# Kernel optimization log

Measured on AMD Instinct MI355X. Metric: run time of the kernel, lower is better.

The kernel has to match this reference:

```python
import jax, jax.numpy as jnp
import numpy as np

BN_EPS = 1e-5


def _weight_mlp(off, Wh, bh, Wo, bo):
    # off: [Nout, k, 2] relative neighbor offsets -> [Nout, k, 9] interp coeffs
    h = jax.nn.relu(off @ Wh + bh)
    return h @ Wo + bo


def _interp_conv(x, idx, off, Wk, bk, Wh, bh, Wo, bo):
    # x: [B, Cin, Nin]; idx: [Nout, k] neighbor indices into Nin; Wk: [Cout, Cin, 9]
    a = _weight_mlp(off, Wh, bh, Wo, bo)        # [Nout, k, 9]
    feats = x[:, :, idx]                         # gather -> [B, Cin, Nout, k]
    # dynamic filter: per-neighbor kernel = a @ Wk taps, contracted with features
    y = jnp.einsum('nkt,bcnk,oct->bon', a, feats, Wk)  # [B, Cout, Nout]
    return y + bk[None, :, None]


def _bn_relu(x, g, b):
    # BatchNorm1d over [B, C, N] using batch statistics (training-mode forward)
    mean = x.mean(axis=(0, 2), keepdims=True)
    var = x.var(axis=(0, 2), keepdims=True)
    xn = (x - mean) * jax.lax.rsqrt(var + BN_EPS)
    return jax.nn.relu(xn * g[None, :, None] + b[None, :, None])


def setup_inputs() -> dict:
    key = jax.random.key(0)
    ks = jax.random.split(key, 12)
    B, N1, N2, N3, K = 8, 50176, 12544, 3136, 9
    inp = {
        'x': jax.random.normal(ks[0], (B, 3, N1), jnp.float32),
        'nbr1': jax.random.randint(ks[1], (N2, K), 0, N1, jnp.int32),
        'off1': jax.random.normal(ks[2], (N2, K, 2), jnp.float32),
        'nbr2': jax.random.randint(ks[3], (N2, K), 0, N2, jnp.int32),
        'off2': jax.random.normal(ks[4], (N2, K, 2), jnp.float32),
        'pool_idx': jax.random.randint(ks[5], (N3, K), 0, N2, jnp.int32),
        'Wh': jax.random.normal(ks[6], (2, 32), jnp.float32) * 0.5,
        'bh': jnp.zeros((32,), jnp.float32),
        'Wo': jax.random.normal(ks[7], (32, 9), jnp.float32) * 0.2,
        'bo': jnp.zeros((9,), jnp.float32),
        'W1': jax.random.normal(ks[8], (32, 3, 9), jnp.float32) * 0.2,
        'b1': jnp.zeros((32,), jnp.float32),
        'W2': jax.random.normal(ks[9], (32, 32, 9), jnp.float32) * 0.06,
        'b2': jnp.zeros((32,), jnp.float32),
        'W3': jax.random.normal(ks[10], (64, 32, 9), jnp.float32) * 0.06,
        'b3': jnp.zeros((64,), jnp.float32),
        'g1': jnp.ones((32,), jnp.float32), 'be1': jnp.zeros((32,), jnp.float32),
        'g2': jnp.ones((32,), jnp.float32), 'be2': jnp.zeros((32,), jnp.float32),
        'g3': jnp.ones((64,), jnp.float32), 'be3': jnp.zeros((64,), jnp.float32),
    }
    return inp


def reference(x, nbr1, off1, nbr2, off2, pool_idx, Wh, bh, Wo, bo,
              W1, b1, W2, b2, W3, b3, g1, be1, g2, be2, g3, be3):
    x = _bn_relu(_interp_conv(x, nbr1, off1, W1, b1, Wh, bh, Wo, bo), g1, be1)
    x = _bn_relu(_interp_conv(x, nbr2, off2, W2, b2, Wh, bh, Wo, bo), g2, be2)
    x = _bn_relu(_interp_conv(x, nbr2, off2, W3, b3, Wh, bh, Wo, bo), g3, be3)
    # MaxPoolNG: max over irregular neighbor sets from level l2 -> l3
    x = x[:, :, pool_idx].max(axis=-1)           # [B, 64, N3]
    return x
```

## Files before the change

kernel.cpp:

```cpp
#include <hip/hip_runtime.h>
#include <math.h>

#define N1C 50176
#define N2C 12544
#define N3C 3136
#define NT_TILES (N2C * 8 / 64)

typedef __attribute__((ext_vector_type(8))) short bf16x8;
typedef __attribute__((ext_vector_type(4))) float f32x4;

__device__ __forceinline__ unsigned short f2bf(float f) {
    unsigned u = __builtin_bit_cast(unsigned, f);
    u += 0x7fffu + ((u >> 16) & 1u);
    return (unsigned short)(u >> 16);
}
__device__ __forceinline__ unsigned packbf(float a, float b) {
    return (unsigned)f2bf(a) | ((unsigned)f2bf(b) << 16);
}
__device__ __forceinline__ float bf2f(unsigned short u) {
    return __builtin_bit_cast(float, (unsigned)u << 16);
}
__device__ __forceinline__ float bflo(unsigned u) {
    return __builtin_bit_cast(float, u << 16);
}
__device__ __forceinline__ float bfhi(unsigned u) {
    return __builtin_bit_cast(float, u & 0xffff0000u);
}

#define TRB (N1C / 64)
#define MLB (2 * N2C * 9 / 256)
#define PWB 112

__device__ __forceinline__ void pad_one(int i, const float* __restrict__ W,
                                        unsigned short* __restrict__ Wp,
                                        int OC, int CIN, int KT) {
    int j = i & 7;
    int op = (i >> 3) & 31;
    int q = (i >> 8) & 3;
    int kt = (i >> 10) % KT;
    int g = i / (KT * 1024);
    int kp = kt * 32 + q * 8 + j;
    int t = kp / CIN, c = kp - t * CIN;
    int o = g * 32 + op;
    float v = (t < 9 && o < OC) ? W[(o * CIN + c) * 9 + t] : 0.f;
    Wp[i] = f2bf(v);
}

__global__ void prologue_kernel(const float* __restrict__ x, unsigned short* __restrict__ X0,
                                const float* __restrict__ off1, const float* __restrict__ off2,
                                const float* __restrict__ Wh, const float* __restrict__ bh,
                                const float* __restrict__ Wo, const float* __restrict__ bo,
                                float* __restrict__ A1, float* __restrict__ A2,
                                const float* __restrict__ W1, const float* __restrict__ W2,
                                const float* __restrict__ W3,
                                unsigned short* __restrict__ W1p, unsigned short* __restrict__ W2p,
                                unsigned short* __restrict__ W3p) {
    __shared__ float T[64][25];
    int blk = blockIdx.x;
    int tid = threadIdx.x;
    if (blk < TRB) {
        int n0 = blk * 64;
        for (int r = tid; r < 24 * 64; r += 256) {
            int cb = r >> 6;
            int nn = r & 63;
            T[nn][cb] = x[cb * N1C + n0 + nn];
        }
        __syncthreads();
        for (int w = tid; w < 64 * 24; w += 256) {
            int nn = w / 24;
            int u = w - nn * 24;
            X0[(n0 + nn) * 24 + u] = f2bf(T[nn][u]);
        }
    } else if (blk < TRB + MLB) {
        int idx = (blk - TRB) * 256 + tid;
        const float* offp;
        float* Ap;
        if (idx < N2C * 9) { offp = off1 + idx * 2; Ap = A1 + idx * 9; }
        else { int i2 = idx - N2C * 9; offp = off2 + i2 * 2; Ap = A2 + i2 * 9; }
        float o0 = offp[0], o1 = offp[1];
        float out[9];
#pragma unroll
        for (int t = 0; t < 9; t++) out[t] = bo[t];
#pragma unroll
        for (int h = 0; h < 32; h++) {
            float hv = fmaxf(o0 * Wh[h] + o1 * Wh[32 + h] + bh[h], 0.f);
#pragma unroll
            for (int t = 0; t < 9; t++) out[t] += hv * Wo[h * 9 + t];
        }
#pragma unroll
        for (int t = 0; t < 9; t++) Ap[t] = out[t];
    } else {
        int i = (blk - TRB - MLB) * 256 + tid;
        if (i < 1024) pad_one(i, W1, W1p, 32, 3, 1);
        else if (i < 10240) pad_one(i - 1024, W2, W2p, 32, 32, 9);
        else pad_one(i - 10240, W3, W3p, 64, 32, 9);
    }
}

template <int CIN, int MW, bool HAS_BN>
__global__ __launch_bounds__(256, 4)
void conv_kernel(const unsigned short* __restrict__ Xin,
                 const int* __restrict__ nbr,
                 const float* __restrict__ A,
                 const unsigned short* __restrict__ Wp,
                 const float* __restrict__ bias,
                 const float* __restrict__ bnsc,
                 const float* __restrict__ bnsh,
                 unsigned short* __restrict__ Yb,
                 double* __restrict__ Part) {
    constexpr int OC = MW * 16;
    constexpr int KREAL = 9 * CIN;
    constexpr int KROW = (KREAL + 31) & ~31;
    constexpr int KT = KROW / 32;
    constexpr int KSTR = KROW + 8;
    __shared__ alignas(16) short S[64 * KSTR];

    int tid = threadIdx.x;
    int tile = blockIdx.x;
    int n0 = tile * 8;

    if constexpr (KROW != KREAL) {
        for (int i = tid; i < 64 * KSTR; i += 256) S[i] = 0;
        __syncthreads();
    }

    if constexpr (CIN == 3) {
        if (tid < 192) {
            int nsub = tid / 24;
            int u = tid - nsub * 24;
            int b = u / 3, c = u - b * 3;
            int n = n0 + nsub;
            const int* nb = nbr + n * 9;
            const float* Ar = A + n * 81;
            float s[9];
#pragma unroll
            for (int t = 0; t < 9; t++) s[t] = 0.f;
#pragma unroll
            for (int k = 0; k < 9; k++) {
                float f = bf2f(Xin[nb[k] * 24 + u]);
#pragma unroll
                for (int t = 0; t < 9; t++) s[t] = fmaf(Ar[k * 9 + t], f, s[t]);
            }
            int col = nsub * 8 + b;
#pragma unroll
            for (int t = 0; t < 9; t++) S[col * KSTR + t * 3 + c] = (short)f2bf(s[t]);
        }
    } else {
        int nhalf = __builtin_amdgcn_readfirstlane(tid >> 7);
        int rem = tid & 127;
        int b = rem >> 4, c2 = rem & 15;
        float sc0 = 1.f, sh0 = 0.f, sc1 = 1.f, sh1 = 0.f;
        if (HAS_BN) {
            sc0 = bnsc[2 * c2];     sc1 = bnsc[2 * c2 + 1];
            sh0 = bnsh[2 * c2];     sh1 = bnsh[2 * c2 + 1];
        }
        const unsigned* Xu = (const unsigned*)Xin;
        int nbase = n0 + nhalf * 4;
        unsigned fu[36];
#pragma unroll
        for (int g = 0; g < 4; g++)
#pragma unroll
            for (int k = 0; k < 9; k++) {
                int j = nbr[(nbase + g) * 9 + k];
                fu[g * 9 + k] = Xu[(size_t)j * 128 + rem];
            }
#pragma unroll
        for (int g = 0; g < 4; g++) {
            const float* Ar = A + (nbase + g) * 81;
            float s0[9], s1[9];
#pragma unroll
            for (int t = 0; t < 9; t++) { s0[t] = 0.f; s1[t] = 0.f; }
#pragma unroll
            for (int k = 0; k < 9; k++) {
                unsigned u = fu[g * 9 + k];
                float lo = bflo(u), hi = bfhi(u);
                if (HAS_BN) {
                    lo = fmaxf(fmaf(lo, sc0, sh0), 0.f);
                    hi = fmaxf(fmaf(hi, sc1, sh1), 0.f);
                }
#pragma unroll
                for (int t = 0; t < 9; t++) {
                    float a = Ar[k * 9 + t];
                    s0[t] = fmaf(a, lo, s0[t]);
                    s1[t] = fmaf(a, hi, s1[t]);
                }
            }
            int col = (nhalf * 4 + g) * 8 + b;
            unsigned* Srow = (unsigned*)&S[col * KSTR];
#pragma unroll
            for (int t = 0; t < 9; t++) Srow[t * 16 + c2] = packbf(s0[t], s1[t]);
        }
    }
    __syncthreads();

    int lane = tid & 63, wv = tid >> 6, q = lane >> 4, cl = lane & 15;
    int colg = wv * 16 + cl;

    const bf16x8* wf = (const bf16x8*)Wp;
    f32x4 acc[MW];
#pragma unroll
    for (int m = 0; m < MW; m++) acc[m] = (f32x4){0.f, 0.f, 0.f, 0.f};
#pragma unroll
    for (int kt = 0; kt < KT; kt++) {
        bf16x8 bfr = *(const bf16x8*)&S[colg * KSTR + kt * 32 + q * 8];
#pragma unroll
        for (int m = 0; m < MW; m++) {
            const bf16x8* wg = wf + (m >> 1) * (KT * 128);
            bf16x8 am = wg[(kt * 4 + q) * 32 + cl + (m & 1) * 16];
            acc[m] = __builtin_amdgcn_mfma_f32_16x16x32_bf16(am, bfr, acc[m], 0, 0, 0);
        }
    }
    __syncthreads();
    double (*redd)[2 * OC] = (double(*)[2 * OC])S;

    int C = tile * 64 + colg;
    float yv[4 * MW];
#pragma unroll
    for (int m = 0; m < MW; m++)
#pragma unroll
        for (int i = 0; i < 4; i++) {
            int o = m * 16 + q * 4 + i;
            float y = acc[m][i] + bias[o];
            yv[m * 4 + i] = y;
            Yb[(size_t)C * OC + o] = f2bf(y);
        }
#pragma unroll
    for (int r = 0; r < 4 * MW; r++) {
        double ps = (double)yv[r];
        double pq = (double)yv[r] * (double)yv[r];
#pragma unroll
        for (int d = 1; d < 16; d <<= 1) {
            ps += __shfl_xor(ps, d);
            pq += __shfl_xor(pq, d);
        }
        if (cl == 0) {
            int o = (r >> 2) * 16 + q * 4 + (r & 3);
            redd[wv][o] = ps;
            redd[wv][OC + o] = pq;
        }
    }
    __syncthreads();
    if (tid < 2 * OC) {
        double v = redd[0][tid] + redd[1][tid] + redd[2][tid] + redd[3][tid];
        Part[(size_t)tid * NT_TILES + tile] = v;
    }
}

__global__ __launch_bounds__(256, 8)
void bn_reduce(const double* __restrict__ Part,
               const float* __restrict__ g, const float* __restrict__ be,
               float* __restrict__ sc, float* __restrict__ sh, int OC) {
    int o = blockIdx.x;
    int tid = threadIdx.x;
    const double* ps = Part + (size_t)o * NT_TILES;
    const double* pq = Part + (size_t)(OC + o) * NT_TILES;
    double s = 0.0, q = 0.0;
    for (int t = tid; t < NT_TILES; t += 256) {
        s += ps[t];
        q += pq[t];
    }
#pragma unroll
    for (int d = 1; d < 64; d <<= 1) {
        s += __shfl_xor(s, d);
        q += __shfl_xor(q, d);
    }
    __shared__ double red[8];
    int wv = tid >> 6;
    if ((tid & 63) == 0) { red[wv] = s; red[4 + wv] = q; }
    __syncthreads();
    if (tid == 0) {
        double S = red[0] + red[1] + red[2] + red[3];
        double Q = red[4] + red[5] + red[6] + red[7];
        double cnt = (double)N2C * 8.0;
        double mean = S / cnt;
        double var = Q / cnt - mean * mean;
        double rs = 1.0 / sqrt(var + 1e-5);
        double scale = (double)g[o] * rs;
        sc[o] = (float)scale;
        sh[o] = (float)((double)be[o] - mean * scale);
    }
}

__global__ __launch_bounds__(512, 4)
void pool_kernel(const unsigned short* __restrict__ Y3, const int* __restrict__ pidx,
                 const float* __restrict__ sc, const float* __restrict__ sh,
                 float* __restrict__ out) {
    int m0 = blockIdx.x * 8;
    int tid = threadIdx.x;
    int o = tid & 63;
    float s = sc[o], h = sh[o];
    float mx[8];
    int jn[9];
#pragma unroll
    for (int k = 0; k < 9; k++) jn[k] = pidx[m0 * 9 + k];
#pragma unroll 1
    for (int mi = 0; mi < 8; mi++) {
        int jc[9];
#pragma unroll
        for (int k = 0; k < 9; k++) jc[k] = jn[k];
        if (mi < 7) {
#pragma unroll
            for (int k = 0; k < 9; k++) jn[k] = pidx[(m0 + mi + 1) * 9 + k];
        }
        float v0 = 0.f;
#pragma unroll
        for (int k = 0; k < 9; k++) {
            float v = bf2f(Y3[(size_t)jc[k] * 512 + tid]);
            v0 = fmaxf(v0, fmaf(v, s, h));
        }
        mx[mi] = fmaxf(v0, 0.f);
    }
    float* op = out + (size_t)tid * 3136 + m0;
#pragma unroll
    for (int mi = 0; mi < 8; mi++) op[mi] = mx[mi];
}

extern "C" void kernel_launch(void* const* d_in, const int* in_sizes, int n_in,
                              void* d_out, int out_size, void* d_ws, size_t ws_size,
                              hipStream_t stream) {
    const float* x    = (const float*)d_in[0];
    const int*   nbr1 = (const int*)d_in[1];
    const float* off1 = (const float*)d_in[2];
    const int*   nbr2 = (const int*)d_in[3];
    const float* off2 = (const float*)d_in[4];
    const int*   pidx = (const int*)d_in[5];
    const float* Wh   = (const float*)d_in[6];
    const float* bh   = (const float*)d_in[7];
    const float* Wo   = (const float*)d_in[8];
    const float* bo   = (const float*)d_in[9];
    const float* W1   = (const float*)d_in[10];
    const float* b1   = (const float*)d_in[11];
    const float* W2   = (const float*)d_in[12];
    const float* b2   = (const float*)d_in[13];
    const float* W3   = (const float*)d_in[14];
    const float* b3   = (const float*)d_in[15];
    const float* g1   = (const float*)d_in[16];
    const float* be1  = (const float*)d_in[17];
    const float* g2   = (const float*)d_in[18];
    const float* be2  = (const float*)d_in[19];
    const float* g3   = (const float*)d_in[20];
    const float* be3  = (const float*)d_in[21];

    char* ws = (char*)d_ws;
    size_t off = 0;
    auto alloc = [&](size_t bytes) -> void* {
        void* p = ws + off;
        off += (bytes + 255) & ~(size_t)255;
        return p;
    };
    unsigned short* X0b = (unsigned short*)alloc((size_t)N1C * 24 * 2);
    float* A1 = (float*)alloc((size_t)N2C * 81 * 4);
    float* A2 = (float*)alloc((size_t)N2C * 81 * 4);
    unsigned short* Y1b = (unsigned short*)alloc((size_t)N2C * 8 * 32 * 2);
    unsigned short* Y2b = (unsigned short*)alloc((size_t)N2C * 8 * 32 * 2);
    unsigned short* Y3b = (unsigned short*)alloc((size_t)N2C * 8 * 64 * 2);
    unsigned short* W1p = (unsigned short*)alloc(32 * 32 * 2);
    unsigned short* W2p = (unsigned short*)alloc(32 * 288 * 2);
    unsigned short* W3p = (unsigned short*)alloc(64 * 288 * 2);
    double* Part  = (double*)alloc((size_t)NT_TILES * 128 * 8);
    float*  scbuf = (float*)alloc(256 * 4);

    float* sc1 = scbuf;       float* sh1 = scbuf + 32;
    float* sc2 = scbuf + 64;  float* sh2 = scbuf + 96;
    float* sc3 = scbuf + 128; float* sh3 = scbuf + 192;

    prologue_kernel<<<TRB + MLB + PWB, 256, 0, stream>>>(
        x, X0b, off1, off2, Wh, bh, Wo, bo, A1, A2, W1, W2, W3, W1p, W2p, W3p);

    conv_kernel<3, 2, false><<<NT_TILES, 256, 0, stream>>>(
        X0b, nbr1, A1, W1p, b1, nullptr, nullptr, Y1b, Part);
    bn_reduce<<<32, 256, 0, stream>>>(Part, g1, be1, sc1, sh1, 32);

    conv_kernel<32, 2, true><<<NT_TILES, 256, 0, stream>>>(
        Y1b, nbr2, A2, W2p, b2, sc1, sh1, Y2b, Part);
    bn_reduce<<<32, 256, 0, stream>>>(Part, g2, be2, sc2, sh2, 32);

    conv_kernel<32, 4, true><<<NT_TILES, 256, 0, stream>>>(
        Y2b, nbr2, A2, W3p, b3, sc2, sh2, Y3b, Part);
    bn_reduce<<<64, 256, 0, stream>>>(Part, g3, be3, sc3, sh3, 64);

    pool_kernel<<<N3C / 8, 512, 0, stream>>>(Y3b, pidx, sc3, sh3, (float*)d_out);
}
```

Baseline: 215.7 us.

## Widen gather loads, pack output stores, use float partial sums, restructure pool

The conv gather now has each lane load 4 bf16 channels at once (uint2) across 4 waves of 2 points each, replacing 2-channel loads per lane, and writes packed 4-channel LDS rows. The epilogue stores 4 bf16 outputs as one 8-byte write and does the shuffle reductions for BN statistics in float instead of double, widening to double only for the final cross-wave sum. The pool kernel is remapped to 2 output points per 256-thread block with 2 channels per lane, so all loads are issued up front and results go out as float2 stores. Float shuffle sums are cheaper than double ones but slightly reduce precision of the variance accumulation.

```diff
diff --git a/kernel.cpp b/kernel.cpp
--- a/kernel.cpp
+++ b/kernel.cpp
@@ -93,7 +93,7 @@
         int i = (blk - TRB - MLB) * 256 + tid;
         if (i < 1024) pad_one(i, W1, W1p, 32, 3, 1);
         else if (i < 10240) pad_one(i - 1024, W2, W2p, 32, 32, 9);
-        else pad_one(i - 10240, W3, W3p, 64, 32, 9);
+        else pad_one(i - 10240, W3, W3p, 64, 288 / 9, 9);
     }
 }
 
@@ -146,49 +146,58 @@
             for (int t = 0; t < 9; t++) S[col * KSTR + t * 3 + c] = (short)f2bf(s[t]);
         }
     } else {
-        int nhalf = __builtin_amdgcn_readfirstlane(tid >> 7);
-        int rem = tid & 127;
-        int b = rem >> 4, c2 = rem & 15;
-        float sc0 = 1.f, sh0 = 0.f, sc1 = 1.f, sh1 = 0.f;
+        int wv4 = __builtin_amdgcn_readfirstlane(tid >> 6);
+        int lane = tid & 63;
+        int b = lane >> 3, c4 = lane & 7;
+        float4 scv = {1.f, 1.f, 1.f, 1.f}, shv = {0.f, 0.f, 0.f, 0.f};
         if (HAS_BN) {
-            sc0 = bnsc[2 * c2];     sc1 = bnsc[2 * c2 + 1];
-            sh0 = bnsh[2 * c2];     sh1 = bnsh[2 * c2 + 1];
-        }
-        const unsigned* Xu = (const unsigned*)Xin;
-        int nbase = n0 + nhalf * 4;
-        unsigned fu[36];
-#pragma unroll
-        for (int g = 0; g < 4; g++)
+            scv = *(const float4*)&bnsc[4 * c4];
+            shv = *(const float4*)&bnsh[4 * c4];
+        }
+        const uint2* Xd = (const uint2*)Xin;
+        uint2 fu[18];
+#pragma unroll
+        for (int gg = 0; gg < 2; gg++)
 #pragma unroll
             for (int k = 0; k < 9; k++) {
-                int j = nbr[(nbase + g) * 9 + k];
-                fu[g * 9 + k] = Xu[(size_t)j * 128 + rem];
+                int j = nbr[(n0 + wv4 * 2 + gg) * 9 + k];
+                fu[gg * 9 + k] = Xd[(size_t)j * 64 + lane];
             }
 #pragma unroll
-        for (int g = 0; g < 4; g++) {
-            const float* Ar = A + (nbase + g) * 81;
-            float s0[9], s1[9];
-#pragma unroll
-            for (int t = 0; t < 9; t++) { s0[t] = 0.f; s1[t] = 0.f; }
+        for (int gg = 0; gg < 2; gg++) {
+            const float* Ar = A + (size_t)(n0 + wv4 * 2 + gg) * 81;
+            float s0[9], s1[9], s2[9], s3[9];
+#pragma unroll
+            for (int t = 0; t < 9; t++) { s0[t] = 0.f; s1[t] = 0.f; s2[t] = 0.f; s3[t] = 0.f; }
 #pragma unroll
             for (int k = 0; k < 9; k++) {
-                unsigned u = fu[g * 9 + k];
-                float lo = bflo(u), hi = bfhi(u);
+                uint2 u = fu[gg * 9 + k];
+                float f0 = bflo(u.x), f1 = bfhi(u.x);
+                float f2 = bflo(u.y), f3 = bfhi(u.y);
                 if (HAS_BN) {
-                    lo = fmaxf(fmaf(lo, sc0, sh0), 0.f);
-                    hi = fmaxf(fmaf(hi, sc1, sh1), 0.f);
+                    f0 = fmaxf(fmaf(f0, scv.x, shv.x), 0.f);
+                    f1 = fmaxf(fmaf(f1, scv.y, shv.y), 0.f);
+                    f2 = fmaxf(fmaf(f2, scv.z, shv.z), 0.f);
+                    f3 = fmaxf(fmaf(f3, scv.w, shv.w), 0.f);
                 }
 #pragma unroll
                 for (int t = 0; t < 9; t++) {
                     float a = Ar[k * 9 + t];
-                    s0[t] = fmaf(a, lo, s0[t]);
-                    s1[t] = fmaf(a, hi, s1[t]);
+                    s0[t] = fmaf(a, f0, s0[t]);
+                    s1[t] = fmaf(a, f1, s1[t]);
+                    s2[t] = fmaf(a, f2, s2[t]);
+                    s3[t] = fmaf(a, f3, s3[t]);
                 }
             }
-            int col = (nhalf * 4 + g) * 8 + b;
-            unsigned* Srow = (unsigned*)&S[col * KSTR];
-#pragma unroll
-            for (int t = 0; t < 9; t++) Srow[t * 16 + c2] = packbf(s0[t], s1[t]);
+            int col = (wv4 * 2 + gg) * 8 + b;
+            uint2* Srow = (uint2*)&S[col * KSTR];
+#pragma unroll
+            for (int t = 0; t < 9; t++) {
+                uint2 pk;
+                pk.x = packbf(s0[t], s1[t]);
+                pk.y = packbf(s2[t], s3[t]);
+                Srow[t * 8 + c4] = pk;
+            }
         }
     }
     __syncthreads();
@@ -211,23 +220,26 @@
         }
     }
     __syncthreads();
-    double (*redd)[2 * OC] = (double(*)[2 * OC])S;
+    float (*redf)[2 * OC] = (float(*)[2 * OC])S;
 
     int C = tile * 64 + colg;
     float yv[4 * MW];
 #pragma unroll
-    for (int m = 0; m < MW; m++)
+    for (int m = 0; m < MW; m++) {
 #pragma unroll
         for (int i = 0; i < 4; i++) {
             int o = m * 16 + q * 4 + i;
-            float y = acc[m][i] + bias[o];
-            yv[m * 4 + i] = y;
-            Yb[(size_t)C * OC + o] = f2bf(y);
-        }
+            yv[m * 4 + i] = acc[m][i] + bias[o];
+        }
+        uint2 pk;
+        pk.x = packbf(yv[m * 4 + 0], yv[m * 4 + 1]);
+        pk.y = packbf(yv[m * 4 + 2], yv[m * 4 + 3]);
+        *(uint2*)&Yb[(size_t)C * OC + m * 16 + q * 4] = pk;
+    }
 #pragma unroll
     for (int r = 0; r < 4 * MW; r++) {
-        double ps = (double)yv[r];
-        double pq = (double)yv[r] * (double)yv[r];
+        float ps = yv[r];
+        float pq = yv[r] * yv[r];
 #pragma unroll
         for (int d = 1; d < 16; d <<= 1) {
             ps += __shfl_xor(ps, d);
@@ -235,13 +247,14 @@
         }
         if (cl == 0) {
             int o = (r >> 2) * 16 + q * 4 + (r & 3);
-            redd[wv][o] = ps;
-            redd[wv][OC + o] = pq;
+            redf[wv][o] = ps;
+            redf[wv][OC + o] = pq;
         }
     }
     __syncthreads();
     if (tid < 2 * OC) {
-        double v = redd[0][tid] + redd[1][tid] + redd[2][tid] + redd[3][tid];
+        double v = (double)redf[0][tid] + (double)redf[1][tid] +
+                   (double)redf[2][tid] + (double)redf[3][tid];
         Part[(size_t)tid * NT_TILES + tile] = v;
     }
 }
@@ -281,38 +294,40 @@
     }
 }
 
-__global__ __launch_bounds__(512, 4)
+__global__ __launch_bounds__(256, 8)
 void pool_kernel(const unsigned short* __restrict__ Y3, const int* __restrict__ pidx,
                  const float* __restrict__ sc, const float* __restrict__ sh,
                  float* __restrict__ out) {
-    int m0 = blockIdx.x * 8;
+    int m0 = blockIdx.x * 2;
     int tid = threadIdx.x;
-    int o = tid & 63;
-    float s = sc[o], h = sh[o];
-    float mx[8];
-    int jn[9];
-#pragma unroll
-    for (int k = 0; k < 9; k++) jn[k] = pidx[m0 * 9 + k];
-#pragma unroll 1
-    for (int mi = 0; mi < 8; mi++) {
-        int jc[9];
-#pragma unroll
-        for (int k = 0; k < 9; k++) jc[k] = jn[k];
-        if (mi < 7) {
-#pragma unroll
-            for (int k = 0; k < 9; k++) jn[k] = pidx[(m0 + mi + 1) * 9 + k];
-        }
-        float v0 = 0.f;
-#pragma unroll
-        for (int k = 0; k < 9; k++) {
-            float v = bf2f(Y3[(size_t)jc[k] * 512 + tid]);
-            v0 = fmaxf(v0, fmaf(v, s, h));
-        }
-        mx[mi] = fmaxf(v0, 0.f);
-    }
-    float* op = out + (size_t)tid * 3136 + m0;
-#pragma unroll
-    for (int mi = 0; mi < 8; mi++) op[mi] = mx[mi];
+    int o2 = tid & 31;
+    int b = tid >> 5;
+    float s0 = sc[2 * o2], h0 = sh[2 * o2];
+    float s1 = sc[2 * o2 + 1], h1 = sh[2 * o2 + 1];
+    const unsigned* Y3u = (const unsigned*)Y3;
+    int j0[9], j1[9];
+#pragma unroll
+    for (int k = 0; k < 9; k++) {
+        j0[k] = pidx[m0 * 9 + k];
+        j1[k] = pidx[m0 * 9 + 9 + k];
+    }
+    unsigned u0[9], u1[9];
+#pragma unroll
+    for (int k = 0; k < 9; k++) u0[k] = Y3u[(size_t)j0[k] * 256 + tid];
+#pragma unroll
+    for (int k = 0; k < 9; k++) u1[k] = Y3u[(size_t)j1[k] * 256 + tid];
+    float a0 = 0.f, a1 = 0.f, c0 = 0.f, c1 = 0.f;
+#pragma unroll
+    for (int k = 0; k < 9; k++) {
+        a0 = fmaxf(a0, fmaf(bflo(u0[k]), s0, h0));
+        a1 = fmaxf(a1, fmaf(bfhi(u0[k]), s1, h1));
+        c0 = fmaxf(c0, fmaf(bflo(u1[k]), s0, h0));
+        c1 = fmaxf(c1, fmaf(bfhi(u1[k]), s1, h1));
+    }
+    float2 r0 = {a0, c0};
+    float2 r1 = {a1, c1};
+    *(float2*)(out + (size_t)(b * 64 + 2 * o2) * 3136 + m0) = r0;
+    *(float2*)(out + (size_t)(b * 64 + 2 * o2 + 1) * 3136 + m0) = r1;
 }
 
 extern "C" void kernel_launch(void* const* d_in, const int* in_sizes, int n_in,
@@ -379,5 +394,5 @@
         Y2b, nbr2, A2, W3p, b3, sc2, sh2, Y3b, Part);
     bn_reduce<<<64, 256, 0, stream>>>(Part, g3, be3, sc3, sh3, 64);
 
-    pool_kernel<<<N3C / 8, 512, 0, stream>>>(Y3b, pidx, sc3, sh3, (float*)d_out);
-}
+    pool_kernel<<<N3C / 2, 256, 0, stream>>>(Y3b, pidx, sc3, sh3, (float*)d_out);
+}
```

Result: faster. 192.3 us (-10.8%).
